# Kernel tuning notes

Measured on AMD Instinct MI355X. Metric: run time of the kernel, lower is better.

Reference implementation:

```python
import jax, jax.numpy as jnp
import numpy as np

B, L, D_SEQ, D_GLOBAL = 32, 2048, 1024, 1024
H, DK, DV = 16, 64, 64


def setup_inputs() -> dict:
    key = jax.random.key(0)
    k1, k2, k3, k4, k5 = jax.random.split(key, 5)
    scale = 0.05
    return {
        "X": jax.random.normal(k1, (B, D_GLOBAL), dtype=jnp.float32),
        "S": jax.random.normal(k2, (B, L, D_SEQ), dtype=jnp.float32),
        "Wq": jax.random.normal(k3, (H, D_GLOBAL, DK), dtype=jnp.float32) * scale,
        "Wk": jax.random.normal(k4, (H, D_SEQ, DK), dtype=jnp.float32) * scale,
        "Wv": jax.random.normal(k5, (H, D_SEQ, DV), dtype=jnp.float32) * scale,
    }


def reference(X, S, Wq, Wk, Wv):
    # X: [B, d_global], S: [B, L, d_seq]
    d_key = Wq.shape[-1]
    inv_sqrt_dk = 1.0 / jnp.sqrt(jnp.float32(d_key))
    # Values: gelu (exact, erf-based like tf default) projection -> [B, H, L, DV]
    VS = jax.nn.gelu(jnp.einsum("bld,hdv->bhlv", S, Wv), approximate=False)
    # Single global query per head: tanh projection -> [B, H, DK]
    Q = jnp.tanh(jnp.einsum("bd,hdk->bhk", X, Wq))
    # Keys: tanh projection -> [B, H, L, DK]
    KS = jnp.tanh(jnp.einsum("bld,hdk->bhlk", S, Wk))
    # Attention logits (batched GEMV): [B, H, L]
    logits = jnp.einsum("bhk,bhlk->bhl", Q, KS) * inv_sqrt_dk
    Z = jax.nn.softmax(logits, axis=-1)
    # Weighted sum of values: [B, H, DV] -> flatten to [B, H*DV]
    Y = jnp.einsum("bhl,bhlv->bhv", Z, VS)
    return Y.reshape(Y.shape[0], -1)
```

## Files before the change

kernel.cpp:

```cpp
#include <hip/hip_runtime.h>
#include <math.h>

#define B_   32
#define L_   2048
#define DSEQ 1024
#define DGLB 1024
#define H_   16
#define DK_  64
#define DV_  64
#define LT   64
#define NT   (L_/LT)
#define PSTRIDE 66

#define WC_KSTRIDE 4096
#define WC_HSTRIDE 131072

#define AS1 __attribute__((address_space(1)))
#define AS3 __attribute__((address_space(3)))

using u16    = unsigned short;
using bf16x8 = __attribute__((ext_vector_type(8))) short;
using f32x4  = __attribute__((ext_vector_type(4))) float;

__device__ __forceinline__ u16 f2bf(float x) {
  union { float f; unsigned int u; } v; v.f = x;
  return (u16)((v.u + 0x7fffu + ((v.u >> 16) & 1u)) >> 16);
}

__device__ __forceinline__ float tanh_fast(float x) {
  float e = __builtin_exp2f(x * 2.885390081777927f);
  return 1.f - 2.f/(e + 1.f);
}

__device__ __forceinline__ float erf_fast(float x) {
  float ax = fabsf(x);
  float t  = 1.f/(1.f + 0.3275911f*ax);
  float p  = t*(0.254829592f + t*(-0.284496736f + t*(1.421413741f +
             t*(-1.453152027f + t*1.061405429f))));
  float e  = __builtin_exp2f(-ax*ax*1.4426950408889634f);
  float r  = 1.f - p*e;
  return copysignf(r, x);
}

#define PHASE_BARRIER(N)                                   \
  do {                                                     \
    __builtin_amdgcn_sched_barrier(0);                     \
    asm volatile("s_waitcnt vmcnt(" #N ")" ::: "memory");  \
    __builtin_amdgcn_s_barrier();                          \
    __builtin_amdgcn_sched_barrier(0);                     \
  } while (0)

__global__ void pack_w_kernel(const float* __restrict__ Wk,
                              const float* __restrict__ Wv,
                              u16* __restrict__ Wc) {
  const int h = blockIdx.x, j = blockIdx.y;
  const float* src = (j < DK_) ? (Wk + (size_t)h*DSEQ*DK_ + j)
                               : (Wv + (size_t)h*DSEQ*DV_ + (j - DK_));
  u16* dst = Wc + (size_t)h*WC_HSTRIDE + (size_t)j*32;
  for (int d = threadIdx.x; d < DSEQ; d += blockDim.x)
    dst[(size_t)(d >> 5)*WC_KSTRIDE + (d & 31)] = f2bf(src[(size_t)d*64]);
}

__global__ void s2bf_kernel(const float* __restrict__ S, u16* __restrict__ Sb) {
  const size_t G = (size_t)B_*L_*DSEQ/8;
  for (size_t i = (size_t)blockIdx.x*256 + threadIdx.x; i < G; i += (size_t)4096*256) {
    const float4* sp = (const float4*)(S + i*8);
    float4 v0 = sp[0], v1 = sp[1];
    bf16x8 wv;
    wv[0]=(short)f2bf(v0.x); wv[1]=(short)f2bf(v0.y);
    wv[2]=(short)f2bf(v0.z); wv[3]=(short)f2bf(v0.w);
    wv[4]=(short)f2bf(v1.x); wv[5]=(short)f2bf(v1.y);
    wv[6]=(short)f2bf(v1.z); wv[7]=(short)f2bf(v1.w);
    *(bf16x8*)(Sb + i*8) = wv;
  }
}

__global__ void q_proj_kernel(const float* __restrict__ X,
                              const float* __restrict__ Wq,
                              float* __restrict__ Q) {
  __shared__ float red[4][4][64];
  const int h = blockIdx.x, b0 = blockIdx.y*4;
  const int k = threadIdx.x & 63, dd = threadIdx.x >> 6;
  const float* w = Wq + (size_t)h*DGLB*DK_ + (size_t)dd*256*DK_ + k;
  float a0=0.f, a1=0.f, a2=0.f, a3=0.f;
  for (int d = 0; d < 256; ++d) {
    float wv = w[(size_t)d*DK_];
    a0 += X[(size_t)(b0+0)*DGLB + dd*256 + d]*wv;
    a1 += X[(size_t)(b0+1)*DGLB + dd*256 + d]*wv;
    a2 += X[(size_t)(b0+2)*DGLB + dd*256 + d]*wv;
    a3 += X[(size_t)(b0+3)*DGLB + dd*256 + d]*wv;
  }
  red[dd][0][k]=a0; red[dd][1][k]=a1; red[dd][2][k]=a2; red[dd][3][k]=a3;
  __syncthreads();
  if (dd == 0) {
    #pragma unroll
    for (int bb = 0; bb < 4; ++bb) {
      float s = red[0][bb][k]+red[1][bb][k]+red[2][bb][k]+red[3][bb][k];
      Q[((size_t)(b0+bb)*H_+h)*DK_+k] = tanhf(s);
    }
  }
}

template<int BF16SRC>
__global__ __launch_bounds__(256, 4) void fused_kernel(
    const float* __restrict__ S, const u16* __restrict__ Sb,
    const u16* __restrict__ Wc, const float* __restrict__ Q,
    float* __restrict__ part) {
  __shared__ u16   Slds[2*64*128];
  __shared__ float lpart[2][64];

  const int id   = blockIdx.x;
  const int xcd  = id & 7;
  const int jg   = xcd >> 1;
  const int cpar = xcd & 1;
  const int idx  = id >> 3;
  const int psel = idx & 1;
  const int mm   = idx >> 1;
  const int pair = 2*jg + psel;
  const int tile = (((mm + (jg << 7)) & 511) << 1) | cpar;
  const int t    = tile & (NT-1), b = tile >> 5;

  const int tid  = threadIdx.x;
  const int wave = tid >> 6, lane = tid & 63;
  const int lhi  = lane >> 4, llo = lane & 15;
  const int isV  = wave & 1,  hp  = wave >> 1;
  const int h    = pair*2 + hp;

  const u16* wb = Wc + (size_t)h*WC_HSTRIDE + (size_t)(isV*64 + llo)*32 + lhi*8;
  int arow[4];
  #pragma unroll
  for (int rt = 0; rt < 4; ++rt) arow[rt] = (rt*16 + llo)*256;

  const u16*   Sv = Sb + ((size_t)b*L_ + (size_t)t*LT)*DSEQ;
  const float* Sf = S  + ((size_t)b*L_ + (size_t)t*LT)*DSEQ;

  auto stage_gl = [&](int sub) {
    const int bs = (sub & 1) * 8192;
    const int ko = (sub & 7) * 128;
    #pragma unroll
    for (int it = 0; it < 4; ++it) {
      const int jj  = wave*4 + it;
      const int row = 4*jj + (lane >> 4);
      const int g   = (lane & 15) ^ (row & 15);
      const u16* gp = Sv + (size_t)row*DSEQ + ko + (g << 3);
      __builtin_amdgcn_global_load_lds(
          (const AS1 void*)gp, (AS3 void*)(Slds + bs + jj*512), 16, 0, 0);
    }
  };
  auto stage_reg = [&](int sub) {
    const int bs = (sub & 1) * 16384;
    const int ko = (sub & 7) * 128;
    #pragma unroll
    for (int it = 0; it < 4; ++it) {
      int f = it*256 + tid, row = f >> 4, q = f & 15;
      int g = q ^ (row & 15);
      const float4* sp = (const float4*)(Sf + (size_t)row*DSEQ + ko + g*8);
      float4 v0 = sp[0], v1 = sp[1];
      bf16x8 wv;
      wv[0]=(short)f2bf(v0.x); wv[1]=(short)f2bf(v0.y);
      wv[2]=(short)f2bf(v0.z); wv[3]=(short)f2bf(v0.w);
      wv[4]=(short)f2bf(v1.x); wv[5]=(short)f2bf(v1.y);
      wv[6]=(short)f2bf(v1.z); wv[7]=(short)f2bf(v1.w);
      *(bf16x8*)((char*)Slds + bs + row*256 + q*16) = wv;
    }
  };

  f32x4 acc[4][4];
  #pragma unroll
  for (int rt = 0; rt < 4; ++rt)
    #pragma unroll
    for (int cc = 0; cc < 4; ++cc) acc[rt][cc] = {0.f,0.f,0.f,0.f};

  if (BF16SRC) {
    stage_gl(0);
    __builtin_amdgcn_sched_barrier(0);
  }
  bf16x8 bA[4], bB[4];
  #pragma unroll
  for (int cc = 0; cc < 4; ++cc) bA[cc] = *(const bf16x8*)(wb + (size_t)0*WC_KSTRIDE + cc*512);
  #pragma unroll
  for (int cc = 0; cc < 4; ++cc) bB[cc] = *(const bf16x8*)(wb + (size_t)1*WC_KSTRIDE + cc*512);
  const u16* wbp = wb + (size_t)2*WC_KSTRIDE;
  if (BF16SRC) PHASE_BARRIER(8);

#define KSTEP(BUF, kk)                                                        \
  do {                                                                        \
    const int colb = (((kk)*4 + lhi) ^ llo) << 4;                             \
    __builtin_amdgcn_s_setprio(1);                                            \
    _Pragma("unroll")                                                         \
    for (int rt = 0; rt < 4; ++rt) {                                          \
      bf16x8 af = *(const bf16x8*)(cb + arow[rt] + colb);                     \
      acc[rt][0] = __builtin_amdgcn_mfma_f32_16x16x32_bf16(af, BUF[0], acc[rt][0], 0,0,0); \
      acc[rt][1] = __builtin_amdgcn_mfma_f32_16x16x32_bf16(af, BUF[1], acc[rt][1], 0,0,0); \
      acc[rt][2] = __builtin_amdgcn_mfma_f32_16x16x32_bf16(af, BUF[2], acc[rt][2], 0,0,0); \
      acc[rt][3] = __builtin_amdgcn_mfma_f32_16x16x32_bf16(af, BUF[3], acc[rt][3], 0,0,0); \
    }                                                                         \
    __builtin_amdgcn_s_setprio(0);                                            \
    {                                                                         \
      _Pragma("unroll")                                                       \
      for (int cc = 0; cc < 4; ++cc)                                          \
        BUF[cc] = *(const bf16x8*)(wbp + cc*512);                             \
      wbp += ((s*4 + (kk) + 2) == 31) ? -(ptrdiff_t)(31*WC_KSTRIDE)           \
                                      : (ptrdiff_t)WC_KSTRIDE;                \
    }                                                                         \
  } while (0)

  #pragma unroll
  for (int s = 0; s < 8; ++s) {
    if (BF16SRC) {
      if (s < 7) { stage_gl(s + 1); __builtin_amdgcn_sched_barrier(0); }
    } else {
      stage_reg(s);
      __syncthreads();
    }
    const char* cb = (const char*)Slds + (s & 1)*16384;
    KSTEP(bA, 0); KSTEP(bB, 1); KSTEP(bA, 2); KSTEP(bB, 3);
    if (BF16SRC) {
      if (s < 7) PHASE_BARRIER(16);
    } else {
      __syncthreads();
    }
  }
#undef KSTEP

  if (!isV) {
    const float* Qb = Q + ((size_t)b*H_ + h)*DK_;
    float q[4];
    #pragma unroll
    for (int cc = 0; cc < 4; ++cc) q[cc] = Qb[16*cc + llo];
    #pragma unroll
    for (int rt = 0; rt < 4; ++rt) {
      #pragma unroll
      for (int r = 0; r < 4; ++r) {
        float pl = q[0]*tanh_fast(acc[rt][0][r]) + q[1]*tanh_fast(acc[rt][1][r])
                 + q[2]*tanh_fast(acc[rt][2][r]) + q[3]*tanh_fast(acc[rt][3][r]);
        pl += __shfl_xor(pl, 1); pl += __shfl_xor(pl, 2);
        pl += __shfl_xor(pl, 4); pl += __shfl_xor(pl, 8);
        if (llo == 0) lpart[hp][rt*16 + lhi*4 + r] = pl;
      }
    }
  } else {
    #pragma unroll
    for (int rt = 0; rt < 4; ++rt)
      #pragma unroll
      for (int cc = 0; cc < 4; ++cc)
        #pragma unroll
        for (int r = 0; r < 4; ++r) {
          float x = acc[rt][cc][r];
          acc[rt][cc][r] = 0.5f*x*(1.f + erf_fast(x*0.70710678118654752f));
        }
  }
  __syncthreads();

  if (isV) {
    float lg = lpart[hp][lane] * 0.125f;
    float mx = lg;
    #pragma unroll
    for (int mk = 1; mk < 64; mk <<= 1) mx = fmaxf(mx, __shfl_xor(mx, mk));
    float ev = __expf(lg - mx);
    float sv = ev;
    #pragma unroll
    for (int mk = 1; mk < 64; mk <<= 1) sv += __shfl_xor(sv, mk);

    float er[16];
    #pragma unroll
    for (int rt = 0; rt < 4; ++rt)
      #pragma unroll
      for (int r = 0; r < 4; ++r)
        er[rt*4 + r] = __shfl(ev, rt*16 + lhi*4 + r);

    float* pt = part + (((size_t)b*H_ + h)*NT + t)*PSTRIDE;
    #pragma unroll
    for (int cc = 0; cc < 4; ++cc) {
      float y = 0.f;
      #pragma unroll
      for (int rt = 0; rt < 4; ++rt)
        #pragma unroll
        for (int r = 0; r < 4; ++r)
          y += er[rt*4 + r]*acc[rt][cc][r];
      y += __shfl_xor(y, 16); y += __shfl_xor(y, 32);
      if (lhi == 0) pt[2 + 16*cc + llo] = y;
    }
    if (lane == 0) { pt[0] = mx; pt[1] = sv; }
  }
}

__global__ void finalize_kernel(const float* __restrict__ part,
                                float* __restrict__ out) {
  const int h = blockIdx.x, b = blockIdx.y, v = threadIdx.x;
  const float* p = part + ((size_t)b*H_ + h)*(size_t)NT*PSTRIDE;
  float M = -3.0e38f;
  for (int tt = 0; tt < NT; ++tt) M = fmaxf(M, p[tt*PSTRIDE]);
  float ss = 0.f, y = 0.f;
  for (int tt = 0; tt < NT; ++tt) {
    float w = expf(p[tt*PSTRIDE] - M);
    ss += w*p[tt*PSTRIDE + 1];
    y  += w*p[tt*PSTRIDE + 2 + v];
  }
  out[((size_t)b*H_ + h)*DV_ + v] = y/ss;
}

extern "C" void kernel_launch(void* const* d_in, const int* in_sizes, int n_in,
                              void* d_out, int out_size, void* d_ws, size_t ws_size,
                              hipStream_t stream) {
  const float* X  = (const float*)d_in[0];
  const float* S  = (const float*)d_in[1];
  const float* Wq = (const float*)d_in[2];
  const float* Wk = (const float*)d_in[3];
  const float* Wv = (const float*)d_in[4];
  float* out = (float*)d_out;

  char* ws = (char*)d_ws;
  u16*   Wc    = (u16*)ws;
  float* Qbuf  = (float*)(ws + (4u<<20));
  float* part  = (float*)(ws + (4u<<20) + (128u<<10));
  u16*   Sb    = (u16*)(ws + (16u<<20));
  const bool useBf = ws_size >= (144ull << 20);

  pack_w_kernel  <<<dim3(H_, 128),  256, 0, stream>>>(Wk, Wv, Wc);
  q_proj_kernel  <<<dim3(H_, B_/4), 256, 0, stream>>>(X, Wq, Qbuf);
  if (useBf) {
    s2bf_kernel       <<<dim3(4096), 256, 0, stream>>>(S, Sb);
    fused_kernel<1>   <<<dim3(8192), 256, 0, stream>>>(S, Sb, Wc, Qbuf, part);
  } else {
    fused_kernel<0>   <<<dim3(8192), 256, 0, stream>>>(S, Sb, Wc, Qbuf, part);
  }
  finalize_kernel<<<dim3(H_, B_),    64, 0, stream>>>(part, out);
}
```

Baseline: 416.9 us.

## Give each wave a full head computing both K and V projections

Each wave now owns one head and computes both the key and value projections, using 8 accumulator column tiles instead of 4. A block covers 4 heads instead of 2, so the grid halves and each staged S tile in LDS feeds twice as many MFMAs, which halves total S reads. The cost is doubled accumulator and B-fragment registers, with launch bounds lowered to 2 blocks per SIMD. Occupancy drops accordingly, and the later phases now run tanh and gelu in every wave.

```diff
diff --git a/kernel.cpp b/kernel.cpp
--- a/kernel.cpp
+++ b/kernel.cpp
@@ -102,31 +102,27 @@
 }
 
 template<int BF16SRC>
-__global__ __launch_bounds__(256, 4) void fused_kernel(
+__global__ __launch_bounds__(256, 2) void fused_kernel(
     const float* __restrict__ S, const u16* __restrict__ Sb,
     const u16* __restrict__ Wc, const float* __restrict__ Q,
     float* __restrict__ part) {
   __shared__ u16   Slds[2*64*128];
-  __shared__ float lpart[2][64];
+  __shared__ float lpart[4][64];
 
   const int id   = blockIdx.x;
   const int xcd  = id & 7;
-  const int jg   = xcd >> 1;
+  const int g    = xcd >> 1;
   const int cpar = xcd & 1;
-  const int idx  = id >> 3;
-  const int psel = idx & 1;
-  const int mm   = idx >> 1;
-  const int pair = 2*jg + psel;
-  const int tile = (((mm + (jg << 7)) & 511) << 1) | cpar;
+  const int mm   = id >> 3;
+  const int tile = (((mm + (g << 7)) & 511) << 1) | cpar;
   const int t    = tile & (NT-1), b = tile >> 5;
 
   const int tid  = threadIdx.x;
   const int wave = tid >> 6, lane = tid & 63;
   const int lhi  = lane >> 4, llo = lane & 15;
-  const int isV  = wave & 1,  hp  = wave >> 1;
-  const int h    = pair*2 + hp;
-
-  const u16* wb = Wc + (size_t)h*WC_HSTRIDE + (size_t)(isV*64 + llo)*32 + lhi*8;
+  const int h    = g*4 + wave;
+
+  const u16* wb = Wc + (size_t)h*WC_HSTRIDE + (size_t)llo*32 + lhi*8;
   int arow[4];
   #pragma unroll
   for (int rt = 0; rt < 4; ++rt) arow[rt] = (rt*16 + llo)*256;
@@ -141,8 +137,8 @@
     for (int it = 0; it < 4; ++it) {
       const int jj  = wave*4 + it;
       const int row = 4*jj + (lane >> 4);
-      const int g   = (lane & 15) ^ (row & 15);
-      const u16* gp = Sv + (size_t)row*DSEQ + ko + (g << 3);
+      const int gg  = (lane & 15) ^ (row & 15);
+      const u16* gp = Sv + (size_t)row*DSEQ + ko + (gg << 3);
       __builtin_amdgcn_global_load_lds(
           (const AS1 void*)gp, (AS3 void*)(Slds + bs + jj*512), 16, 0, 0);
     }
@@ -153,8 +149,8 @@
     #pragma unroll
     for (int it = 0; it < 4; ++it) {
       int f = it*256 + tid, row = f >> 4, q = f & 15;
-      int g = q ^ (row & 15);
-      const float4* sp = (const float4*)(Sf + (size_t)row*DSEQ + ko + g*8);
+      int gg = q ^ (row & 15);
+      const float4* sp = (const float4*)(Sf + (size_t)row*DSEQ + ko + gg*8);
       float4 v0 = sp[0], v1 = sp[1];
       bf16x8 wv;
       wv[0]=(short)f2bf(v0.x); wv[1]=(short)f2bf(v0.y);
@@ -165,23 +161,23 @@
     }
   };
 
-  f32x4 acc[4][4];
+  f32x4 acc[4][8];
   #pragma unroll
   for (int rt = 0; rt < 4; ++rt)
     #pragma unroll
-    for (int cc = 0; cc < 4; ++cc) acc[rt][cc] = {0.f,0.f,0.f,0.f};
+    for (int cc = 0; cc < 8; ++cc) acc[rt][cc] = {0.f,0.f,0.f,0.f};
 
   if (BF16SRC) {
     stage_gl(0);
     __builtin_amdgcn_sched_barrier(0);
   }
-  bf16x8 bA[4], bB[4];
-  #pragma unroll
-  for (int cc = 0; cc < 4; ++cc) bA[cc] = *(const bf16x8*)(wb + (size_t)0*WC_KSTRIDE + cc*512);
-  #pragma unroll
-  for (int cc = 0; cc < 4; ++cc) bB[cc] = *(const bf16x8*)(wb + (size_t)1*WC_KSTRIDE + cc*512);
+  bf16x8 bA[8], bB[8];
+  #pragma unroll
+  for (int cc = 0; cc < 8; ++cc) bA[cc] = *(const bf16x8*)(wb + (size_t)0*WC_KSTRIDE + cc*512);
+  #pragma unroll
+  for (int cc = 0; cc < 8; ++cc) bB[cc] = *(const bf16x8*)(wb + (size_t)1*WC_KSTRIDE + cc*512);
   const u16* wbp = wb + (size_t)2*WC_KSTRIDE;
-  if (BF16SRC) PHASE_BARRIER(8);
+  if (BF16SRC) PHASE_BARRIER(16);
 
 #define KSTEP(BUF, kk)                                                        \
   do {                                                                        \
@@ -190,15 +186,14 @@
     _Pragma("unroll")                                                         \
     for (int rt = 0; rt < 4; ++rt) {                                          \
       bf16x8 af = *(const bf16x8*)(cb + arow[rt] + colb);                     \
-      acc[rt][0] = __builtin_amdgcn_mfma_f32_16x16x32_bf16(af, BUF[0], acc[rt][0], 0,0,0); \
-      acc[rt][1] = __builtin_amdgcn_mfma_f32_16x16x32_bf16(af, BUF[1], acc[rt][1], 0,0,0); \
-      acc[rt][2] = __builtin_amdgcn_mfma_f32_16x16x32_bf16(af, BUF[2], acc[rt][2], 0,0,0); \
-      acc[rt][3] = __builtin_amdgcn_mfma_f32_16x16x32_bf16(af, BUF[3], acc[rt][3], 0,0,0); \
+      _Pragma("unroll")                                                       \
+      for (int cc = 0; cc < 8; ++cc)                                          \
+        acc[rt][cc] = __builtin_amdgcn_mfma_f32_16x16x32_bf16(af, BUF[cc], acc[rt][cc], 0,0,0); \
     }                                                                         \
     __builtin_amdgcn_s_setprio(0);                                            \
     {                                                                         \
       _Pragma("unroll")                                                       \
-      for (int cc = 0; cc < 4; ++cc)                                          \
+      for (int cc = 0; cc < 8; ++cc)                                          \
         BUF[cc] = *(const bf16x8*)(wbp + cc*512);                             \
       wbp += ((s*4 + (kk) + 2) == 31) ? -(ptrdiff_t)(31*WC_KSTRIDE)           \
                                       : (ptrdiff_t)WC_KSTRIDE;                \
@@ -216,14 +211,14 @@
     const char* cb = (const char*)Slds + (s & 1)*16384;
     KSTEP(bA, 0); KSTEP(bB, 1); KSTEP(bA, 2); KSTEP(bB, 3);
     if (BF16SRC) {
-      if (s < 7) PHASE_BARRIER(16);
+      if (s < 7) PHASE_BARRIER(32);
     } else {
       __syncthreads();
     }
   }
 #undef KSTEP
 
-  if (!isV) {
+  {
     const float* Qb = Q + ((size_t)b*H_ + h)*DK_;
     float q[4];
     #pragma unroll
@@ -236,24 +231,23 @@
                  + q[2]*tanh_fast(acc[rt][2][r]) + q[3]*tanh_fast(acc[rt][3][r]);
         pl += __shfl_xor(pl, 1); pl += __shfl_xor(pl, 2);
         pl += __shfl_xor(pl, 4); pl += __shfl_xor(pl, 8);
-        if (llo == 0) lpart[hp][rt*16 + lhi*4 + r] = pl;
+        if (llo == 0) lpart[wave][rt*16 + lhi*4 + r] = pl;
       }
     }
-  } else {
-    #pragma unroll
-    for (int rt = 0; rt < 4; ++rt)
+  }
+  #pragma unroll
+  for (int rt = 0; rt < 4; ++rt)
+    #pragma unroll
+    for (int cc = 4; cc < 8; ++cc)
       #pragma unroll
-      for (int cc = 0; cc < 4; ++cc)
-        #pragma unroll
-        for (int r = 0; r < 4; ++r) {
-          float x = acc[rt][cc][r];
-          acc[rt][cc][r] = 0.5f*x*(1.f + erf_fast(x*0.70710678118654752f));
-        }
-  }
+      for (int r = 0; r < 4; ++r) {
+        float x = acc[rt][cc][r];
+        acc[rt][cc][r] = 0.5f*x*(1.f + erf_fast(x*0.70710678118654752f));
+      }
   __syncthreads();
 
-  if (isV) {
-    float lg = lpart[hp][lane] * 0.125f;
+  {
+    float lg = lpart[wave][lane] * 0.125f;
     float mx = lg;
     #pragma unroll
     for (int mk = 1; mk < 64; mk <<= 1) mx = fmaxf(mx, __shfl_xor(mx, mk));
@@ -277,7 +271,7 @@
       for (int rt = 0; rt < 4; ++rt)
         #pragma unroll
         for (int r = 0; r < 4; ++r)
-          y += er[rt*4 + r]*acc[rt][cc][r];
+          y += er[rt*4 + r]*acc[rt][cc + 4][r];
       y += __shfl_xor(y, 16); y += __shfl_xor(y, 32);
       if (lhi == 0) pt[2 + 16*cc + llo] = y;
     }
@@ -321,9 +315,9 @@
   q_proj_kernel  <<<dim3(H_, B_/4), 256, 0, stream>>>(X, Wq, Qbuf);
   if (useBf) {
     s2bf_kernel       <<<dim3(4096), 256, 0, stream>>>(S, Sb);
-    fused_kernel<1>   <<<dim3(8192), 256, 0, stream>>>(S, Sb, Wc, Qbuf, part);
+    fused_kernel<1>   <<<dim3(4096), 256, 0, stream>>>(S, Sb, Wc, Qbuf, part);
   } else {
-    fused_kernel<0>   <<<dim3(8192), 256, 0, stream>>>(S, Sb, Wc, Qbuf, part);
+    fused_kernel<0>   <<<dim3(4096), 256, 0, stream>>>(S, Sb, Wc, Qbuf, part);
   }
   finalize_kernel<<<dim3(H_, B_),    64, 0, stream>>>(part, out);
 }
```

Measured after the change: 413.8 us. No clear change (-0.7%).
